# Kernel tuning notes

Hardware: AMD Instinct MI355X
Metric: run time of the kernel (lower is better)

The kernel has to match this reference:

```python
import jax, jax.numpy as jnp
import numpy as np

CN = 64  # cn_base

def conv2d(x, w, b):
    y = jax.lax.conv_general_dilated(x, w, (1, 1), 'SAME', dimension_numbers=('NCHW', 'OIHW', 'NCHW'))
    return y + b[None, :, None, None]

def epipolar_unfold(feat, xy, bw):
    # feat [B,C,h,w], xy [B,np,el,2] int (x,y) -> [B,C,(2bw+1)*el,np]
    B, C, h, w = feat.shape
    npx, el = xy.shape[1], xy.shape[2]
    dy = jnp.arange(-bw, bw + 1)                                   # band offsets [K]
    y = jnp.clip(xy[..., 1][..., None] + dy, 0, h - 1)             # [B,np,el,K]
    x = jnp.clip(xy[..., 0], 0, w - 1)[..., None]                  # [B,np,el,1]
    idx = (y * w + x).reshape(B, -1)                               # [B,np*el*K]
    out = jnp.take_along_axis(feat.reshape(B, C, h * w), idx[:, None, :], axis=2)
    out = out.reshape(B, C, npx, el * (2 * bw + 1))
    return jnp.transpose(out, (0, 1, 3, 2))                        # [B,C,nsz,np]

def setup_inputs():
    key = jax.random.key(0)
    ks = jax.random.split(key, 20)
    b, ns, c, h, w, el, D, bw = 1, 4, 3, 64, 64, 8, 8, 1
    npx = h * w
    nsz = (2 * bw + 1) * el
    cn_emb = (ns - 1) * 2 + 3 * CN + 2 + 6  # 206
    rn = lambda i, shp, s=1.0: jax.random.normal(ks[i], shp, jnp.float32) * s
    return {
        'source_views': rn(0, (b, ns, c, h, w)),
        'source_flows': rn(1, (b, ns, ns - 1, 2, h, w)),
        'psvs': rn(2, (b, ns, c, D, h, w)),
        'warped_source_views': rn(3, (b, ns, ns - 1, c, h, w)),
        'source_posemaps': rn(4, (b, ns, 6)),
        'neighbor_xy': jax.random.randint(ks[5], (b, ns, npx, el, 2), 0, w, jnp.int32),
        'spa_code': rn(6, (b, ns, 2, nsz, npx)),
        'ang_code': rn(7, (b, ns, 6, nsz, npx)),
        'band_width': bw,
        'flow_w': rn(8, (CN, (ns - 1) * 2 + c + (ns - 1) * c, 3, 3), 0.02),
        'flow_b': rn(9, (CN,), 0.02),
        'ctx_w': rn(10, (CN, c, 3, 3), 0.02),
        'ctx_b': rn(11, (CN,), 0.02),
        'wnet_w': rn(12, (cn_emb, 1), 0.02),
        'wnet_b': rn(13, (1,), 0.02),
        'cnet_w': rn(14, (cn_emb, 1), 0.02),
        'cnet_b': rn(15, (1,), 0.02),
        'psv_w': rn(16, (CN, 2 * c, 3, 3), 0.02),
        'psv_b': rn(17, (CN,), 0.02),
        'vref_w': rn(18, (c, c + 2 * ns * CN, 3, 3), 0.02),
        'vref_b': rn(19, (c,), 0.02),
    }

def reference(source_views, source_flows, psvs, warped_source_views, source_posemaps,
              neighbor_xy, spa_code, ang_code, band_width,
              flow_w, flow_b, ctx_w, ctx_b, wnet_w, wnet_b, cnet_w, cnet_b,
              psv_w, psv_b, vref_w, vref_b):
    b, ns, c, h, w = source_views.shape
    npx, el = neighbor_xy.shape[2], neighbor_xy.shape[3]
    ps = int(round(npx ** 0.5))
    D = psvs.shape[3]
    bw = int(band_width)
    nsz = (2 * bw + 1) * el
    B = b * ns
    sv = source_views.reshape(B, c, h, w)
    sf = source_flows.reshape(B, (ns - 1) * 2, h, w)
    wv = warped_source_views.reshape(B, (ns - 1) * c, h, w)
    nxy = neighbor_xy.reshape(B, npx, el, 2)
    spa = spa_code.reshape(B, 2, nsz, npx)
    ang = ang_code.reshape(B, 6, nsz, npx)
    # sub-networks (flowRefNet / ctxNet)
    ce = jax.nn.relu(conv2d(jnp.concatenate([sf, sv, wv], axis=1), flow_w, flow_b))  # [B,64,h,w]
    ctx = jax.nn.relu(conv2d(sv, ctx_w, ctx_b))                                      # [B,64,h,w]
    # epipolar gathers -> [B,C,nsz,np]
    sv_u = epipolar_unfold(sv, nxy, bw)
    ctx_u = epipolar_unfold(ctx, nxy, bw)
    ce_u = epipolar_unfold(ce, nxy, bw)
    sf_u = epipolar_unfold(sf, nxy, bw)
    mu = jnp.broadcast_to(jnp.mean(ce_u, axis=2, keepdims=True), ce_u.shape)
    var = jnp.broadcast_to(jnp.var(ce_u, axis=2, keepdims=True, ddof=1), ce_u.shape)
    emb = jnp.concatenate([sf_u, ce_u, mu, var, spa, ang], axis=1)   # [B,206,nsz,np]
    # weightNet: per-pixel softmax weight over neighbor_size
    emb_t = jnp.transpose(emb, (0, 3, 2, 1))                          # [B,np,nsz,206]
    weight = jax.nn.softmax((emb_t @ wnet_w)[..., 0] + wnet_b[0], axis=-1)  # [B,np,nsz]
    w_sg = jax.lax.stop_gradient(weight)
    interp_view = jnp.einsum('bcnp,bpn->bpc', sv_u, weight)           # [B,np,c]
    interp_ctx = jnp.einsum('bknp,bpn->bpk', ctx_u, w_sg)             # [B,np,64]
    interp_emb = jnp.einsum('bknp,bpn->bpk', emb, w_sg)               # [B,np,206]
    # confNet: softmax confidence over sources
    ie = jnp.transpose(interp_emb.reshape(b, ns, npx, -1), (0, 2, 1, 3))  # [b,np,ns,206]
    confs = jax.nn.softmax((ie @ cnet_w)[..., 0] + cnet_b[0], axis=2)     # [b,np,ns]
    iv4 = interp_view.reshape(b, ns, npx, c)
    blended = jnp.einsum('bspc,bps->bpc', iv4, confs)                 # [b,np,c]
    blended_img = jnp.transpose(blended, (0, 2, 1)).reshape(b, c, ps, ps)
    # psvNet: per depth-slice conv then mean over D
    psv_sl = jnp.transpose(psvs, (0, 1, 3, 2, 4, 5)).reshape(b * ns * D, c, ps, ps)
    bexp = jnp.broadcast_to(blended_img[:, None, None], (b, ns, D, c, ps, ps)).reshape(b * ns * D, c, ps, ps)
    psv_feat = jax.nn.relu(conv2d(jnp.concatenate([psv_sl, bexp], axis=1), psv_w, psv_b))
    psv_feat = psv_feat.reshape(b, ns, D, CN, ps, ps).mean(axis=2)    # [b,ns,64,ps,ps]
    ictx = jnp.transpose(interp_ctx.reshape(b, ns, ps, ps, CN), (0, 1, 4, 2, 3)).reshape(b, ns * CN, ps, ps)
    ref_in = jnp.concatenate([blended_img, ictx, psv_feat.reshape(b, ns * CN, ps, ps)], axis=1)
    ref_novel_view = conv2d(ref_in, vref_w, vref_b)                   # [b,3,ps,ps]
    return (ref_novel_view,
            blended_img,
            jnp.transpose(interp_view.reshape(b, ns, ps, ps, c), (0, 1, 4, 2, 3)),
            weight.reshape(b, ns, ps, ps, nsz),
            jnp.transpose(confs, (0, 2, 1)).reshape(b, ns, ps, ps))
```

## Files before the change

kernel.cpp:

```cpp
#include <hip/hip_runtime.h>
#include <hip/hip_bf16.h>


#define NS   4
#define NPX  4096
#define NSZ  24
#define PS   64
#define VINW 520
#define CW   66

#define OFF0 0
#define OFF1 12288
#define OFF2 24576
#define OFF3 73728
#define OFF4 466944

__device__ unsigned g_cc [NS * NPX * 64];
__device__ float2 g_fld[NS * NPX];
__device__ unsigned short g_vin [NPX * VINW];
__device__ float g_iv  [NS * NPX * 3];
__device__ float g_clg [NS * NPX];
__device__ float g_bl  [3 * NPX];
__device__ float g_fwT [162 * 64];
__device__ float g_cwT [27 * 64];
__device__ float g_pwT [54 * 64];
__device__ unsigned short g_vwT [3 * 9 * VINW];

__device__ __forceinline__ int clampi(int v, int lo, int hi) {
    return v < lo ? lo : (v > hi ? hi : v);
}
__device__ __forceinline__ unsigned bf16_bits(float f) {
    unsigned u = __float_as_uint(f);
    return (u + 0x7fffu + ((u >> 16) & 1u)) >> 16;
}
__device__ __forceinline__ float bf16_lo(unsigned v) { return __uint_as_float(v << 16); }
__device__ __forceinline__ float bf16_hi(unsigned v) { return __uint_as_float(v & 0xffff0000u); }
__device__ __forceinline__ float ldbf(const unsigned short* p, int i) {
    return __uint_as_float(((unsigned)p[i]) << 16);
}

__global__ void k_prep(const float* __restrict__ fw, const float* __restrict__ cw,
                       const float* __restrict__ pw, const float* __restrict__ vw)
{
    const int i = blockIdx.x * 256 + threadIdx.x;
    const int stride = gridDim.x * 256;
    for (int d = i; d < 162 * 64; d += stride) g_fwT[d] = fw[(d & 63) * 162 + (d >> 6)];
    for (int d = i; d < 27 * 64;  d += stride) g_cwT[d] = cw[(d & 63) * 27  + (d >> 6)];
    for (int d = i; d < 54 * 64;  d += stride) g_pwT[d] = pw[(d & 63) * 54  + (d >> 6)];
    for (int d = i; d < 3 * 9 * VINW; d += stride) {
        const int oc = d / (9 * VINW), rem = d % (9 * VINW);
        const int t = rem / VINW, nch = rem % VINW;
        float v = 0.f;
        if (nch < 256)      v = vw[(oc * 515 + 3 + nch) * 9 + t];
        else if (nch < 512) v = vw[(oc * 515 + 259 + (nch - 256)) * 9 + t];
        else if (nch < 515) v = vw[(oc * 515 + (nch - 512)) * 9 + t];
        g_vwT[d] = (unsigned short)bf16_bits(v);
    }
}

__global__ __launch_bounds__(256) void k_convs(
    const float* __restrict__ sv, const float* __restrict__ sf, const float* __restrict__ wv,
    const float* __restrict__ flow_b, const float* __restrict__ ctx_b,
    const float* __restrict__ wnet_w, const float* __restrict__ cnet_w)
{
    __shared__ float lds[18 * 3 * CW];
    const int s  = blockIdx.x >> 6, py = blockIdx.x & 63;
    const int tid = threadIdx.x;

    for (int i = tid; i < 18 * 3 * CW; i += 256) lds[i] = 0.f;
    __syncthreads();
    for (int i = tid; i < 18 * 3 * 64; i += 256) {
        const int col = i & 63;
        const int r   = (i >> 6) % 3;
        const int pl  = i / 192;
        const int iy  = py + r - 1;
        if ((unsigned)iy < 64u) {
            const float* src = (pl < 6) ? (sf + (s * 6 + pl) * NPX)
                             : (pl < 9) ? (sv + (s * 3 + (pl - 6)) * NPX)
                                        : (wv + (s * 9 + (pl - 9)) * NPX);
            lds[(pl * 3 + r) * CW + col + 1] = src[iy * 64 + col];
        }
    }
    __syncthreads();

    const int oc  = tid & 63;
    const int px0 = (tid >> 6) * 16;

    float acc_ce[16], acc_ctx[16];
    const float fb = flow_b[oc], cb = ctx_b[oc];
    #pragma unroll
    for (int j = 0; j < 16; ++j) { acc_ce[j] = fb; acc_ctx[j] = cb; }

    for (int pl = 0; pl < 18; ++pl) {
        float w[9];
        #pragma unroll
        for (int t = 0; t < 9; ++t) w[t] = g_fwT[(pl * 9 + t) * 64 + oc];
        float wc[9];
        const bool has_ctx = (pl >= 6 && pl < 9);
        if (has_ctx) {
            #pragma unroll
            for (int t = 0; t < 9; ++t) wc[t] = g_cwT[((pl - 6) * 9 + t) * 64 + oc];
        }
        float c0[3], c1[3], c2[3];
        #pragma unroll
        for (int r = 0; r < 3; ++r) {
            c0[r] = lds[(pl * 3 + r) * CW + px0];
            c1[r] = lds[(pl * 3 + r) * CW + px0 + 1];
        }
        #pragma unroll
        for (int j = 0; j < 16; ++j) {
            #pragma unroll
            for (int r = 0; r < 3; ++r)
                c2[r] = lds[(pl * 3 + r) * CW + px0 + j + 2];
            float a = 0.f;
            #pragma unroll
            for (int r = 0; r < 3; ++r)
                a += c0[r] * w[r * 3 + 0] + c1[r] * w[r * 3 + 1] + c2[r] * w[r * 3 + 2];
            acc_ce[j] += a;
            if (has_ctx) {
                float b2 = 0.f;
                #pragma unroll
                for (int r = 0; r < 3; ++r)
                    b2 += c0[r] * wc[r * 3 + 0] + c1[r] * wc[r * 3 + 1] + c2[r] * wc[r * 3 + 2];
                acc_ctx[j] += b2;
            }
            #pragma unroll
            for (int r = 0; r < 3; ++r) { c0[r] = c1[r]; c1[r] = c2[r]; }
        }
    }

    const float Wce = wnet_w[6 + oc], Cce = cnet_w[6 + oc];
    float awsel = 0.f, acsel = 0.f;
    #pragma unroll
    for (int j = 0; j < 16; ++j) {
        const float ce = fmaxf(acc_ce[j], 0.f);
        const float cx = fmaxf(acc_ctx[j], 0.f);
        const int p = py * 64 + px0 + j;
        g_cc[(s * NPX + p) * 64 + oc] = bf16_bits(ce) | (bf16_bits(cx) << 16);
        float gw = ce * Wce, gc = ce * Cce;
        #pragma unroll
        for (int off = 32; off; off >>= 1) {
            gw += __shfl_xor(gw, off, 64);
            gc += __shfl_xor(gc, off, 64);
        }
        awsel = (oc == j) ? gw : awsel;
        acsel = (oc == j) ? gc : acsel;
    }
    if (oc < 16) {
        const int px = px0 + oc;
        float fwv = 0.f, fcv = 0.f;
        #pragma unroll
        for (int c = 0; c < 6; ++c) {
            const float v = lds[(c * 3 + 1) * CW + px + 1];
            fwv += v * wnet_w[c];
            fcv += v * cnet_w[c];
        }
        g_fld[s * NPX + py * 64 + px] = make_float2(awsel + fwv, acsel + fcv);
    }
}

__global__ __launch_bounds__(256) void k_epi(
    const float* __restrict__ sv, const int* __restrict__ nxy,
    const float* __restrict__ spa, const float* __restrict__ ang,
    const float* __restrict__ wnet_w, const float* __restrict__ wnet_b,
    const float* __restrict__ cnet_w,
    float* __restrict__ out)
{
    const int blk = blockIdx.x;
    const int wid = threadIdx.x >> 6;
    const int l   = threadIdx.x & 63;
    const int s   = (blk & 7) >> 1;
    const int p   = (blk >> 3) * 8 + (blk & 1) * 4 + wid;

    int q[NSZ];
    #pragma unroll
    for (int e = 0; e < 8; ++e) {
        int nx = nxy[((s * NPX + p) * 8 + e) * 2 + 0];
        int ny = nxy[((s * NPX + p) * 8 + e) * 2 + 1];
        nx = clampi(nx, 0, 63);
        #pragma unroll
        for (int k = 0; k < 3; ++k) {
            int y = clampi(ny + k - 1, 0, 63);
            q[e * 3 + k] = y * 64 + nx;
        }
    }

    const unsigned* ccp = g_cc + (size_t)s * NPX * 64;
    unsigned cc[NSZ];
    #pragma unroll
    for (int n = 0; n < NSZ; ++n) cc[n] = ccp[q[n] * 64 + l];

    float mu = 0.f;
    #pragma unroll
    for (int n = 0; n < NSZ; ++n) mu += bf16_lo(cc[n]);
    mu *= (1.f / 24.f);
    float var = 0.f;
    #pragma unroll
    for (int n = 0; n < NSZ; ++n) { const float d = bf16_lo(cc[n]) - mu; var += d * d; }
    var *= (1.f / 23.f);

    float pw = mu * wnet_w[70 + l] + var * wnet_w[134 + l];
    float pc = mu * cnet_w[70 + l] + var * cnet_w[134 + l];
    #pragma unroll
    for (int off = 32; off; off >>= 1) {
        pw += __shfl_xor(pw, off, 64);
        pc += __shfl_xor(pc, off, 64);
    }
    const float base_w = pw, base_c = pc;

    float Aw = 0.f, Ac = 0.f;
    if (l < NSZ) {
        const float2 A = g_fld[s * NPX + q[l]];
        Aw = A.x; Ac = A.y;
        #pragma unroll
        for (int c = 0; c < 2; ++c) {
            const float v = spa[((s * 2 + c) * NSZ + l) * NPX + p];
            Aw += v * wnet_w[198 + c];
            Ac += v * cnet_w[198 + c];
        }
        #pragma unroll
        for (int c = 0; c < 6; ++c) {
            const float v = ang[((s * 6 + c) * NSZ + l) * NPX + p];
            Aw += v * wnet_w[200 + c];
            Ac += v * cnet_w[200 + c];
        }
    }

    float logit = (l < NSZ) ? (Aw + base_w + wnet_b[0]) : -1e30f;
    float mx = logit;
    #pragma unroll
    for (int off = 32; off; off >>= 1) mx = fmaxf(mx, __shfl_xor(mx, off, 64));
    float e = (l < NSZ) ? __expf(logit - mx) : 0.f;
    float ssum = e;
    #pragma unroll
    for (int off = 32; off; off >>= 1) ssum += __shfl_xor(ssum, off, 64);
    const float wgt = e / ssum;

    float clp = (l < NSZ) ? (Ac + base_c) * wgt : 0.f;
    #pragma unroll
    for (int off = 32; off; off >>= 1) clp += __shfl_xor(clp, off, 64);
    if (l == 0) g_clg[s * NPX + p] = clp;

    if (l < NSZ) out[OFF3 + (s * NPX + p) * NSZ + l] = wgt;

    float wall[NSZ];
    #pragma unroll
    for (int n = 0; n < NSZ; ++n) wall[n] = __shfl(wgt, n, 64);

    float sc = 0.f;
    #pragma unroll
    for (int n = 0; n < NSZ; ++n) sc += bf16_hi(cc[n]) * wall[n];
    g_vin[p * VINW + s * 64 + l] = (unsigned short)bf16_bits(sc);

    if (l < 3) {
        float svv = 0.f;
        #pragma unroll
        for (int n = 0; n < NSZ; ++n) svv += sv[(s * 3 + l) * NPX + q[n]] * wall[n];
        g_iv[(s * NPX + p) * 3 + l] = svv;
        out[OFF2 + (s * 3 + l) * NPX + p] = svv;
    }
}

__global__ __launch_bounds__(64) void k_conf(
    const float* __restrict__ cnet_b, float* __restrict__ out)
{
    const int p = blockIdx.x * 64 + threadIdx.x;
    const float cb = cnet_b[0];

    float lg[NS];
    #pragma unroll
    for (int s = 0; s < NS; ++s) lg[s] = g_clg[s * NPX + p] + cb;
    float m = lg[0];
    #pragma unroll
    for (int s = 1; s < NS; ++s) m = fmaxf(m, lg[s]);
    float ssum = 0.f;
    float conf[NS];
    #pragma unroll
    for (int s = 0; s < NS; ++s) { conf[s] = __expf(lg[s] - m); ssum += conf[s]; }
    const float inv = 1.f / ssum;
    #pragma unroll
    for (int s = 0; s < NS; ++s) {
        conf[s] *= inv;
        out[OFF4 + s * NPX + p] = conf[s];
    }
    #pragma unroll
    for (int c = 0; c < 3; ++c) {
        float acc = 0.f;
        #pragma unroll
        for (int s = 0; s < NS; ++s)
            acc += g_iv[(s * NPX + p) * 3 + c] * conf[s];
        g_bl[c * NPX + p] = acc;
        g_vin[p * VINW + 512 + c] = (unsigned short)bf16_bits(acc);
        out[OFF1 + c * NPX + p] = acc;
    }
}

__global__ __launch_bounds__(256) void k_psv(
    const float* __restrict__ psvs, const float* __restrict__ psv_b)
{
    __shared__ float lds[27 * 3 * CW];
    const int s  = blockIdx.x >> 6, py = blockIdx.x & 63;
    const int tid = threadIdx.x;

    for (int i = tid; i < 27 * 3 * CW; i += 256) lds[i] = 0.f;
    __syncthreads();
    for (int i = tid; i < 27 * 3 * 64; i += 256) {
        const int col = i & 63;
        const int r   = (i >> 6) % 3;
        const int pl  = i / 192;
        const int iy  = py + r - 1;
        if ((unsigned)iy < 64u) {
            const float* src = (pl < 24) ? (psvs + (s * 24 + pl) * NPX)
                                         : (g_bl + (pl - 24) * NPX);
            lds[(pl * 3 + r) * CW + col + 1] = src[iy * 64 + col];
        }
    }
    __syncthreads();

    const int oc  = tid & 63;
    const int px0 = (tid >> 6) * 16;
    const float bias = psv_b[oc];

    float wp[3][9];
    #pragma unroll
    for (int ic = 0; ic < 3; ++ic)
        #pragma unroll
        for (int t = 0; t < 9; ++t) wp[ic][t] = g_pwT[(ic * 9 + t) * 64 + oc];

    float bconst[16];
    #pragma unroll
    for (int j = 0; j < 16; ++j) bconst[j] = bias;
    for (int ic = 0; ic < 3; ++ic) {
        float w[9];
        #pragma unroll
        for (int t = 0; t < 9; ++t) w[t] = g_pwT[((3 + ic) * 9 + t) * 64 + oc];
        const int pl = 24 + ic;
        float c0[3], c1[3], c2[3];
        #pragma unroll
        for (int r = 0; r < 3; ++r) {
            c0[r] = lds[(pl * 3 + r) * CW + px0];
            c1[r] = lds[(pl * 3 + r) * CW + px0 + 1];
        }
        #pragma unroll
        for (int j = 0; j < 16; ++j) {
            #pragma unroll
            for (int r = 0; r < 3; ++r)
                c2[r] = lds[(pl * 3 + r) * CW + px0 + j + 2];
            float a = 0.f;
            #pragma unroll
            for (int r = 0; r < 3; ++r)
                a += c0[r] * w[r * 3 + 0] + c1[r] * w[r * 3 + 1] + c2[r] * w[r * 3 + 2];
            bconst[j] += a;
            #pragma unroll
            for (int r = 0; r < 3; ++r) { c0[r] = c1[r]; c1[r] = c2[r]; }
        }
    }

    float acc[16];
    #pragma unroll
    for (int j = 0; j < 16; ++j) acc[j] = 0.f;

    for (int d = 0; d < 8; ++d) {
        float a[16];
        #pragma unroll
        for (int j = 0; j < 16; ++j) a[j] = bconst[j];
        #pragma unroll
        for (int ic = 0; ic < 3; ++ic) {
            const int pl = ic * 8 + d;
            float c0[3], c1[3], c2[3];
            #pragma unroll
            for (int r = 0; r < 3; ++r) {
                c0[r] = lds[(pl * 3 + r) * CW + px0];
                c1[r] = lds[(pl * 3 + r) * CW + px0 + 1];
            }
            #pragma unroll
            for (int j = 0; j < 16; ++j) {
                #pragma unroll
                for (int r = 0; r < 3; ++r)
                    c2[r] = lds[(pl * 3 + r) * CW + px0 + j + 2];
                float t2 = 0.f;
                #pragma unroll
                for (int r = 0; r < 3; ++r)
                    t2 += c0[r] * wp[ic][r * 3 + 0] + c1[r] * wp[ic][r * 3 + 1] + c2[r] * wp[ic][r * 3 + 2];
                a[j] += t2;
                #pragma unroll
                for (int r = 0; r < 3; ++r) { c0[r] = c1[r]; c1[r] = c2[r]; }
            }
        }
        #pragma unroll
        for (int j = 0; j < 16; ++j) acc[j] += fmaxf(a[j], 0.f);
    }
    #pragma unroll
    for (int j = 0; j < 16; ++j)
        g_vin[(py * 64 + px0 + j) * VINW + 256 + s * 64 + oc] =
            (unsigned short)bf16_bits(acc[j] * 0.125f);
}

__global__ __launch_bounds__(64) void k_vref(
    const float* __restrict__ vref_b, float* __restrict__ out)
{
    const int p = blockIdx.x;
    const int py = p >> 6, px = p & 63;
    const int l = threadIdx.x;

    float acc[3] = {0.f, 0.f, 0.f};
    #pragma unroll
    for (int t = 0; t < 9; ++t) {
        const int iy = py + t / 3 - 1, ix = px + t % 3 - 1;
        if ((unsigned)iy >= 64u || (unsigned)ix >= 64u) continue;
        const int rowbase = (iy * 64 + ix) * VINW;
        const uint4 vv = *(const uint4*)(g_vin + rowbase + 8 * l);
        float v[8];
        v[0] = bf16_lo(vv.x); v[1] = bf16_hi(vv.x);
        v[2] = bf16_lo(vv.y); v[3] = bf16_hi(vv.y);
        v[4] = bf16_lo(vv.z); v[5] = bf16_hi(vv.z);
        v[6] = bf16_lo(vv.w); v[7] = bf16_hi(vv.w);
        #pragma unroll
        for (int oc = 0; oc < 3; ++oc) {
            const uint4 ww = *(const uint4*)(g_vwT + (oc * 9 + t) * VINW + 8 * l);
            acc[oc] += v[0] * bf16_lo(ww.x) + v[1] * bf16_hi(ww.x)
                     + v[2] * bf16_lo(ww.y) + v[3] * bf16_hi(ww.y)
                     + v[4] * bf16_lo(ww.z) + v[5] * bf16_hi(ww.z)
                     + v[6] * bf16_lo(ww.w) + v[7] * bf16_hi(ww.w);
        }
        if (l < 3) {
            const float bv = ldbf(g_vin, rowbase + 512 + l);
            #pragma unroll
            for (int oc = 0; oc < 3; ++oc)
                acc[oc] += bv * ldbf(g_vwT, (oc * 9 + t) * VINW + 512 + l);
        }
    }
    #pragma unroll
    for (int off = 32; off; off >>= 1) {
        #pragma unroll
        for (int oc = 0; oc < 3; ++oc)
            acc[oc] += __shfl_xor(acc[oc], off, 64);
    }
    if (l == 0) {
        #pragma unroll
        for (int oc = 0; oc < 3; ++oc)
            out[OFF0 + oc * NPX + p] = acc[oc] + vref_b[oc];
    }
}

extern "C" void kernel_launch(void* const* d_in, const int* in_sizes, int n_in,
                              void* d_out, int out_size, void* d_ws, size_t ws_size,
                              hipStream_t stream)
{
    auto find1 = [&](int sz, int fb) -> int {
        for (int i = 0; i < n_in; ++i) if (in_sizes[i] == sz) return i;
        return fb;
    };
    const int i_sv  = find1(49152, 0);
    const int i_sf  = find1(98304, 1);
    const int i_psv = find1(393216, 2);
    const int i_wv  = find1(147456, 3);
    const int i_nxy = find1(262144, 5);
    const int i_spa = find1(786432, 6);
    const int i_ang = find1(2359296, 7);
    const int i_fw  = find1(10368, 9);
    const int i_cw  = find1(1728, 11);
    const int i_pw  = find1(3456, 17);
    const int i_vw  = find1(13905, 19);
    const int i_vb  = find1(3, 20);
    int i_ww = -1, i_cnw = -1;
    for (int i = 0; i < n_in; ++i)
        if (in_sizes[i] == 206) { if (i_ww < 0) i_ww = i; else { i_cnw = i; break; } }
    if (i_ww  < 0) i_ww  = 13;
    if (i_cnw < 0) i_cnw = 15;
    int b64[3] = {10, 12, 18}; int c64 = 0;
    for (int i = 0; i < n_in && c64 < 3; ++i) if (in_sizes[i] == 64) b64[c64++] = i;
    const int i_fb = b64[0], i_cb = b64[1], i_pb = b64[2];
    int i_wb = -1, i_cnb = -1;
    for (int i = i_fw + 1; i < n_in; ++i)
        if (in_sizes[i] == 1) { if (i_wb < 0) i_wb = i; else { i_cnb = i; break; } }
    if (i_wb  < 0) i_wb  = 14;
    if (i_cnb < 0) i_cnb = 16;

    const float* sv     = (const float*)d_in[i_sv];
    const float* sf     = (const float*)d_in[i_sf];
    const float* psvs   = (const float*)d_in[i_psv];
    const float* wv     = (const float*)d_in[i_wv];
    const int*   nxy    = (const int*)d_in[i_nxy];
    const float* spa    = (const float*)d_in[i_spa];
    const float* ang    = (const float*)d_in[i_ang];
    const float* flow_w = (const float*)d_in[i_fw];
    const float* flow_b = (const float*)d_in[i_fb];
    const float* ctx_w  = (const float*)d_in[i_cw];
    const float* ctx_b  = (const float*)d_in[i_cb];
    const float* wnet_w = (const float*)d_in[i_ww];
    const float* wnet_b = (const float*)d_in[i_wb];
    const float* cnet_w = (const float*)d_in[i_cnw];
    const float* cnet_b = (const float*)d_in[i_cnb];
    const float* psv_w  = (const float*)d_in[i_pw];
    const float* psv_b  = (const float*)d_in[i_pb];
    const float* vref_w = (const float*)d_in[i_vw];
    const float* vref_b = (const float*)d_in[i_vb];
    (void)d_ws; (void)ws_size; (void)out_size;

    float* out = (float*)d_out;

    k_prep <<<64, 256, 0, stream>>>(flow_w, ctx_w, psv_w, vref_w);
    k_convs<<<256, 256, 0, stream>>>(sv, sf, wv, flow_b, ctx_b, wnet_w, cnet_w);
    k_epi  <<<4096, 256, 0, stream>>>(sv, nxy, spa, ang, wnet_w, wnet_b, cnet_w, out);
    k_conf <<<64, 64, 0, stream>>>(cnet_b, out);
    k_psv  <<<256, 256, 0, stream>>>(psvs, psv_b);
    k_vref <<<4096, 64, 0, stream>>>(vref_b, out);
}
```

Measured before the change: 200.3 us.

## Fuse softmax blend into psv conv and split conv rows into halves

Removes the separate confidence/blend kernel. Each psv block now recomputes the softmax over views and the blended image for its halo tile directly into shared memory, with only one view writing the outputs. Both the context conv and the psv conv now tile by half-rows of 32 pixels, which doubles the grid to 512 blocks and halves the per-thread accumulators. This trades some redundant halo and softmax work across blocks for one fewer launch and better occupancy.

```diff
diff --git a/kernel.cpp b/kernel.cpp
--- a/kernel.cpp
+++ b/kernel.cpp
@@ -7,7 +7,7 @@
 #define NSZ  24
 #define PS   64
 #define VINW 520
-#define CW   66
+#define HW   34
 
 #define OFF0 0
 #define OFF1 12288
@@ -20,7 +20,6 @@
 __device__ unsigned short g_vin [NPX * VINW];
 __device__ float g_iv  [NS * NPX * 3];
 __device__ float g_clg [NS * NPX];
-__device__ float g_bl  [3 * NPX];
 __device__ float g_fwT [162 * 64];
 __device__ float g_cwT [27 * 64];
 __device__ float g_pwT [54 * 64];
@@ -63,33 +62,36 @@
     const float* __restrict__ flow_b, const float* __restrict__ ctx_b,
     const float* __restrict__ wnet_w, const float* __restrict__ cnet_w)
 {
-    __shared__ float lds[18 * 3 * CW];
-    const int s  = blockIdx.x >> 6, py = blockIdx.x & 63;
+    __shared__ float lds[18 * 3 * HW];
+    const int blk = blockIdx.x;
+    const int s = blk >> 7, py = (blk & 127) >> 1, half = blk & 1;
     const int tid = threadIdx.x;
 
-    for (int i = tid; i < 18 * 3 * CW; i += 256) lds[i] = 0.f;
-    __syncthreads();
-    for (int i = tid; i < 18 * 3 * 64; i += 256) {
-        const int col = i & 63;
-        const int r   = (i >> 6) % 3;
-        const int pl  = i / 192;
-        const int iy  = py + r - 1;
-        if ((unsigned)iy < 64u) {
+    for (int i = tid; i < 18 * 3 * HW; i += 256) {
+        const int lc = i % HW;
+        const int rr = (i / HW) % 3;
+        const int pl = i / (3 * HW);
+        const int iy = py + rr - 1;
+        const int ix = half * 32 + lc - 1;
+        float v = 0.f;
+        if ((unsigned)iy < 64u && (unsigned)ix < 64u) {
             const float* src = (pl < 6) ? (sf + (s * 6 + pl) * NPX)
                              : (pl < 9) ? (sv + (s * 3 + (pl - 6)) * NPX)
                                         : (wv + (s * 9 + (pl - 9)) * NPX);
-            lds[(pl * 3 + r) * CW + col + 1] = src[iy * 64 + col];
-        }
+            v = src[iy * 64 + ix];
+        }
+        lds[i] = v;
     }
     __syncthreads();
 
     const int oc  = tid & 63;
-    const int px0 = (tid >> 6) * 16;
-
-    float acc_ce[16], acc_ctx[16];
+    const int wid = tid >> 6;
+    const int lc0 = wid * 8;
+
+    float acc_ce[8], acc_ctx[8];
     const float fb = flow_b[oc], cb = ctx_b[oc];
     #pragma unroll
-    for (int j = 0; j < 16; ++j) { acc_ce[j] = fb; acc_ctx[j] = cb; }
+    for (int j = 0; j < 8; ++j) { acc_ce[j] = fb; acc_ctx[j] = cb; }
 
     for (int pl = 0; pl < 18; ++pl) {
         float w[9];
@@ -104,14 +106,14 @@
         float c0[3], c1[3], c2[3];
         #pragma unroll
         for (int r = 0; r < 3; ++r) {
-            c0[r] = lds[(pl * 3 + r) * CW + px0];
-            c1[r] = lds[(pl * 3 + r) * CW + px0 + 1];
-        }
-        #pragma unroll
-        for (int j = 0; j < 16; ++j) {
+            c0[r] = lds[(pl * 3 + r) * HW + lc0];
+            c1[r] = lds[(pl * 3 + r) * HW + lc0 + 1];
+        }
+        #pragma unroll
+        for (int j = 0; j < 8; ++j) {
             #pragma unroll
             for (int r = 0; r < 3; ++r)
-                c2[r] = lds[(pl * 3 + r) * CW + px0 + j + 2];
+                c2[r] = lds[(pl * 3 + r) * HW + lc0 + j + 2];
             float a = 0.f;
             #pragma unroll
             for (int r = 0; r < 3; ++r)
@@ -132,10 +134,10 @@
     const float Wce = wnet_w[6 + oc], Cce = cnet_w[6 + oc];
     float awsel = 0.f, acsel = 0.f;
     #pragma unroll
-    for (int j = 0; j < 16; ++j) {
+    for (int j = 0; j < 8; ++j) {
         const float ce = fmaxf(acc_ce[j], 0.f);
         const float cx = fmaxf(acc_ctx[j], 0.f);
-        const int p = py * 64 + px0 + j;
+        const int p = py * 64 + half * 32 + wid * 8 + j;
         g_cc[(s * NPX + p) * 64 + oc] = bf16_bits(ce) | (bf16_bits(cx) << 16);
         float gw = ce * Wce, gc = ce * Cce;
         #pragma unroll
@@ -146,16 +148,16 @@
         awsel = (oc == j) ? gw : awsel;
         acsel = (oc == j) ? gc : acsel;
     }
-    if (oc < 16) {
-        const int px = px0 + oc;
+    if (oc < 8) {
+        const int lpx = wid * 8 + oc;
         float fwv = 0.f, fcv = 0.f;
         #pragma unroll
         for (int c = 0; c < 6; ++c) {
-            const float v = lds[(c * 3 + 1) * CW + px + 1];
+            const float v = lds[(c * 3 + 1) * HW + lpx + 1];
             fwv += v * wnet_w[c];
             fcv += v * cnet_w[c];
         }
-        g_fld[s * NPX + py * 64 + px] = make_float2(awsel + fwv, acsel + fcv);
+        g_fld[s * NPX + py * 64 + half * 32 + lpx] = make_float2(awsel + fwv, acsel + fcv);
     }
 }
 
@@ -261,64 +263,75 @@
     }
 }
 
-__global__ __launch_bounds__(64) void k_conf(
+__global__ __launch_bounds__(256) void k_psv(
+    const float* __restrict__ psvs, const float* __restrict__ psv_b,
     const float* __restrict__ cnet_b, float* __restrict__ out)
 {
-    const int p = blockIdx.x * 64 + threadIdx.x;
-    const float cb = cnet_b[0];
-
-    float lg[NS];
-    #pragma unroll
-    for (int s = 0; s < NS; ++s) lg[s] = g_clg[s * NPX + p] + cb;
-    float m = lg[0];
-    #pragma unroll
-    for (int s = 1; s < NS; ++s) m = fmaxf(m, lg[s]);
-    float ssum = 0.f;
-    float conf[NS];
-    #pragma unroll
-    for (int s = 0; s < NS; ++s) { conf[s] = __expf(lg[s] - m); ssum += conf[s]; }
-    const float inv = 1.f / ssum;
-    #pragma unroll
-    for (int s = 0; s < NS; ++s) {
-        conf[s] *= inv;
-        out[OFF4 + s * NPX + p] = conf[s];
-    }
-    #pragma unroll
-    for (int c = 0; c < 3; ++c) {
-        float acc = 0.f;
-        #pragma unroll
-        for (int s = 0; s < NS; ++s)
-            acc += g_iv[(s * NPX + p) * 3 + c] * conf[s];
-        g_bl[c * NPX + p] = acc;
-        g_vin[p * VINW + 512 + c] = (unsigned short)bf16_bits(acc);
-        out[OFF1 + c * NPX + p] = acc;
-    }
-}
-
-__global__ __launch_bounds__(256) void k_psv(
-    const float* __restrict__ psvs, const float* __restrict__ psv_b)
-{
-    __shared__ float lds[27 * 3 * CW];
-    const int s  = blockIdx.x >> 6, py = blockIdx.x & 63;
+    __shared__ float lds[27 * 3 * HW];
+    const int blk = blockIdx.x;
+    const int s = blk >> 7, py = (blk & 127) >> 1, half = blk & 1;
     const int tid = threadIdx.x;
 
-    for (int i = tid; i < 27 * 3 * CW; i += 256) lds[i] = 0.f;
+    for (int i = tid; i < 27 * 3 * HW; i += 256) {
+        const int lc = i % HW;
+        const int rr = (i / HW) % 3;
+        const int pl = i / (3 * HW);
+        float v = 0.f;
+        if (pl < 24) {
+            const int iy = py + rr - 1;
+            const int ix = half * 32 + lc - 1;
+            if ((unsigned)iy < 64u && (unsigned)ix < 64u)
+                v = psvs[(s * 24 + pl) * NPX + iy * 64 + ix];
+        }
+        lds[i] = v;
+    }
     __syncthreads();
-    for (int i = tid; i < 27 * 3 * 64; i += 256) {
-        const int col = i & 63;
-        const int r   = (i >> 6) % 3;
-        const int pl  = i / 192;
-        const int iy  = py + r - 1;
-        if ((unsigned)iy < 64u) {
-            const float* src = (pl < 24) ? (psvs + (s * 24 + pl) * NPX)
-                                         : (g_bl + (pl - 24) * NPX);
-            lds[(pl * 3 + r) * CW + col + 1] = src[iy * 64 + col];
+
+    if (tid < 3 * HW) {
+        const int r = tid / HW, lc = tid % HW;
+        const int iy = py + r - 1, ix = half * 32 + lc - 1;
+        if ((unsigned)iy < 64u && (unsigned)ix < 64u) {
+            const int p = iy * 64 + ix;
+            const float cb = cnet_b[0];
+            float lg[NS];
+            #pragma unroll
+            for (int ss = 0; ss < NS; ++ss) lg[ss] = g_clg[ss * NPX + p] + cb;
+            float m = lg[0];
+            #pragma unroll
+            for (int ss = 1; ss < NS; ++ss) m = fmaxf(m, lg[ss]);
+            float ssum = 0.f;
+            float conf[NS];
+            #pragma unroll
+            for (int ss = 0; ss < NS; ++ss) { conf[ss] = __expf(lg[ss] - m); ssum += conf[ss]; }
+            const float inv = 1.f / ssum;
+            #pragma unroll
+            for (int ss = 0; ss < NS; ++ss) conf[ss] *= inv;
+            float bl[3];
+            #pragma unroll
+            for (int c = 0; c < 3; ++c) {
+                float a = 0.f;
+                #pragma unroll
+                for (int ss = 0; ss < NS; ++ss)
+                    a += g_iv[(ss * NPX + p) * 3 + c] * conf[ss];
+                bl[c] = a;
+                lds[((24 + c) * 3 + r) * HW + lc] = a;
+            }
+            if (s == 0 && r == 1 && lc >= 1 && lc <= 32) {
+                #pragma unroll
+                for (int ss = 0; ss < NS; ++ss) out[OFF4 + ss * NPX + p] = conf[ss];
+                #pragma unroll
+                for (int c = 0; c < 3; ++c) {
+                    out[OFF1 + c * NPX + p] = bl[c];
+                    g_vin[p * VINW + 512 + c] = (unsigned short)bf16_bits(bl[c]);
+                }
+            }
         }
     }
     __syncthreads();
 
     const int oc  = tid & 63;
-    const int px0 = (tid >> 6) * 16;
+    const int wid = tid >> 6;
+    const int lc0 = wid * 8;
     const float bias = psv_b[oc];
 
     float wp[3][9];
@@ -327,9 +340,9 @@
         #pragma unroll
         for (int t = 0; t < 9; ++t) wp[ic][t] = g_pwT[(ic * 9 + t) * 64 + oc];
 
-    float bconst[16];
-    #pragma unroll
-    for (int j = 0; j < 16; ++j) bconst[j] = bias;
+    float bconst[8];
+    #pragma unroll
+    for (int j = 0; j < 8; ++j) bconst[j] = bias;
     for (int ic = 0; ic < 3; ++ic) {
         float w[9];
         #pragma unroll
@@ -338,14 +351,14 @@
         float c0[3], c1[3], c2[3];
         #pragma unroll
         for (int r = 0; r < 3; ++r) {
-            c0[r] = lds[(pl * 3 + r) * CW + px0];
-            c1[r] = lds[(pl * 3 + r) * CW + px0 + 1];
-        }
-        #pragma unroll
-        for (int j = 0; j < 16; ++j) {
+            c0[r] = lds[(pl * 3 + r) * HW + lc0];
+            c1[r] = lds[(pl * 3 + r) * HW + lc0 + 1];
+        }
+        #pragma unroll
+        for (int j = 0; j < 8; ++j) {
             #pragma unroll
             for (int r = 0; r < 3; ++r)
-                c2[r] = lds[(pl * 3 + r) * CW + px0 + j + 2];
+                c2[r] = lds[(pl * 3 + r) * HW + lc0 + j + 2];
             float a = 0.f;
             #pragma unroll
             for (int r = 0; r < 3; ++r)
@@ -356,28 +369,28 @@
         }
     }
 
-    float acc[16];
-    #pragma unroll
-    for (int j = 0; j < 16; ++j) acc[j] = 0.f;
+    float acc[8];
+    #pragma unroll
+    for (int j = 0; j < 8; ++j) acc[j] = 0.f;
 
     for (int d = 0; d < 8; ++d) {
-        float a[16];
-        #pragma unroll
-        for (int j = 0; j < 16; ++j) a[j] = bconst[j];
+        float a[8];
+        #pragma unroll
+        for (int j = 0; j < 8; ++j) a[j] = bconst[j];
         #pragma unroll
         for (int ic = 0; ic < 3; ++ic) {
             const int pl = ic * 8 + d;
             float c0[3], c1[3], c2[3];
             #pragma unroll
             for (int r = 0; r < 3; ++r) {
-                c0[r] = lds[(pl * 3 + r) * CW + px0];
-                c1[r] = lds[(pl * 3 + r) * CW + px0 + 1];
+                c0[r] = lds[(pl * 3 + r) * HW + lc0];
+                c1[r] = lds[(pl * 3 + r) * HW + lc0 + 1];
             }
             #pragma unroll
-            for (int j = 0; j < 16; ++j) {
+            for (int j = 0; j < 8; ++j) {
                 #pragma unroll
                 for (int r = 0; r < 3; ++r)
-                    c2[r] = lds[(pl * 3 + r) * CW + px0 + j + 2];
+                    c2[r] = lds[(pl * 3 + r) * HW + lc0 + j + 2];
                 float t2 = 0.f;
                 #pragma unroll
                 for (int r = 0; r < 3; ++r)
@@ -388,11 +401,11 @@
             }
         }
         #pragma unroll
-        for (int j = 0; j < 16; ++j) acc[j] += fmaxf(a[j], 0.f);
-    }
-    #pragma unroll
-    for (int j = 0; j < 16; ++j)
-        g_vin[(py * 64 + px0 + j) * VINW + 256 + s * 64 + oc] =
+        for (int j = 0; j < 8; ++j) acc[j] += fmaxf(a[j], 0.f);
+    }
+    #pragma unroll
+    for (int j = 0; j < 8; ++j)
+        g_vin[(py * 64 + half * 32 + wid * 8 + j) * VINW + 256 + s * 64 + oc] =
             (unsigned short)bf16_bits(acc[j] * 0.125f);
 }
 
@@ -501,9 +514,8 @@
     float* out = (float*)d_out;
 
     k_prep <<<64, 256, 0, stream>>>(flow_w, ctx_w, psv_w, vref_w);
-    k_convs<<<256, 256, 0, stream>>>(sv, sf, wv, flow_b, ctx_b, wnet_w, cnet_w);
+    k_convs<<<512, 256, 0, stream>>>(sv, sf, wv, flow_b, ctx_b, wnet_w, cnet_w);
     k_epi  <<<4096, 256, 0, stream>>>(sv, nxy, spa, ang, wnet_w, wnet_b, cnet_w, out);
-    k_conf <<<64, 64, 0, stream>>>(cnet_b, out);
-    k_psv  <<<256, 256, 0, stream>>>(psvs, psv_b);
+    k_psv  <<<512, 256, 0, stream>>>(psvs, psv_b, cnet_b, out);
     k_vref <<<4096, 64, 0, stream>>>(vref_b, out);
 }
```

Result: faster. 175.3 us (-12.5%).
